# Kernel optimization log

Measured on AMD Instinct MI355X. Metric: run time of the kernel, lower is better.

Reference implementation:

```python
import jax, jax.numpy as jnp
import numpy as np

C = 512
K = 3
DIL = 1
EPS = 1e-6


def weight_quant(w):
    # BitNet b1.58 ternary quantization with straight-through estimator:
    # scale = mean(|w|); w_q = clamp(round(w/scale), -1, 1) * scale
    s = jnp.maximum(jnp.mean(jnp.abs(w)), 1e-5)
    q = jnp.clip(jnp.round(w / s), -1.0, 1.0) * s
    return w + jax.lax.stop_gradient(q - w)


def conv1d(x, w, b, padding, dilation):
    # x: [B, C, L], w: [O, I, K]
    y = jax.lax.conv_general_dilated(
        x, w, window_strides=(1,), padding=[(padding, padding)],
        rhs_dilation=(dilation,), dimension_numbers=("NCH", "OIH", "NCH"))
    return y + b[None, :, None]


def setup_inputs() -> dict:
    key = jax.random.key(0)
    k0, k1, k2, k3, k4 = jax.random.split(key, 5)
    fan_in = C * K
    lim = 1.0 / np.sqrt(fan_in)
    x = jax.random.normal(k0, (16, C, 4096), dtype=jnp.float32)
    w1 = jax.random.uniform(k1, (C, C, K), jnp.float32, -lim, lim)
    b1 = jax.random.uniform(k2, (C,), jnp.float32, -lim, lim)
    w2 = jax.random.uniform(k3, (C, C, K), jnp.float32, -lim, lim)
    b2 = jax.random.uniform(k4, (C,), jnp.float32, -lim, lim)
    g = jnp.ones((C,), dtype=jnp.float32)  # RMSNorm gain
    return {"x": x, "w1": w1, "b1": b1, "w2": w2, "b2": b2, "g": g}


def reference(x, w1, b1, w2, b2, g):
    residual = x
    # RMSNorm over channel axis (original transposes to [B,L,C], norms last dim)
    ms = jnp.mean(jnp.square(x), axis=1, keepdims=True)
    h = x * jax.lax.rsqrt(ms + EPS) * g[None, :, None]
    h = jax.nn.silu(h)
    p1 = (K * DIL - DIL) // 2
    h = conv1d(h, weight_quant(w1), b1, p1, DIL)
    h = jax.nn.silu(h)
    h = conv1d(h, weight_quant(w2), b2, K // 2, 1)
    return h + residual
```

## Files before the change

### kernel.cpp

```cpp
#include <hip/hip_runtime.h>

#define BATCH 16
#define CCH 512
#define LEN 4096
#define LPAD 4098

typedef unsigned short u16;
typedef __bf16 bf16x8 __attribute__((ext_vector_type(8)));
typedef float f32x4 __attribute__((ext_vector_type(4)));
typedef u16 u16x8 __attribute__((ext_vector_type(8)));
typedef u16 u16x4 __attribute__((ext_vector_type(4)));

__device__ __forceinline__ u16 f2bf(float f) {
    unsigned u = __float_as_uint(f);
    u = (u + 0x7fffu + ((u >> 16) & 1u)) >> 16;
    return (u16)u;
}
__device__ __forceinline__ float bf2f(u16 v) {
    return __uint_as_float(((unsigned)v) << 16);
}
__device__ __forceinline__ float silu_f(float v) {
    return v / (1.f + __expf(-v));
}
__device__ __forceinline__ void async16(const u16* g, u16* l) {
    __builtin_amdgcn_global_load_lds(
        (const __attribute__((address_space(1))) unsigned int*)g,
        (__attribute__((address_space(3))) unsigned int*)l, 16, 0, 0);
}

#define SBAR() __builtin_amdgcn_sched_barrier(0)
#define HWBAR() { SBAR(); __builtin_amdgcn_s_barrier(); SBAR(); }
#define WAIT_LGKM0() { asm volatile("s_waitcnt lgkmcnt(0)" ::: "memory"); SBAR(); }
#define WAIT_VM(n) { asm volatile("s_waitcnt vmcnt(" #n ")" ::: "memory"); SBAR(); }

__global__ __launch_bounds__(256)
void absmean_partial(const float* __restrict__ w1, const float* __restrict__ w2,
                     float* __restrict__ part) {
    const int tid = threadIdx.x;
    const int base = blockIdx.x * 3072;
    float s1 = 0.f, s2 = 0.f;
    for (int i = tid; i < 3072; i += 256) {
        s1 += fabsf(w1[base + i]);
        s2 += fabsf(w2[base + i]);
    }
    __shared__ float r1[256], r2[256];
    r1[tid] = s1; r2[tid] = s2;
    __syncthreads();
    for (int off = 128; off > 0; off >>= 1) {
        if (tid < off) { r1[tid] += r1[tid + off]; r2[tid] += r2[tid + off]; }
        __syncthreads();
    }
    if (tid == 0) { part[blockIdx.x] = r1[0]; part[256 + blockIdx.x] = r2[0]; }
}

__global__ __launch_bounds__(256)
void finalize_scale(const float* __restrict__ part, float* __restrict__ sv) {
    const int tid = threadIdx.x;
    __shared__ float r1[256], r2[256];
    r1[tid] = part[tid]; r2[tid] = part[256 + tid];
    __syncthreads();
    for (int off = 128; off > 0; off >>= 1) {
        if (tid < off) { r1[tid] += r1[tid + off]; r2[tid] += r2[tid + off]; }
        __syncthreads();
    }
    if (tid == 0) {
        sv[0] = fmaxf(r1[0] * (1.f / 786432.f), 1e-5f);
        sv[1] = fmaxf(r2[0] * (1.f / 786432.f), 1e-5f);
    }
}

__global__ __launch_bounds__(256)
void quantize_w(const float* __restrict__ w, const float* __restrict__ sv,
                int sidx, u16* __restrict__ wqt) {
    const int idx = blockIdx.x * 256 + threadIdx.x;
    const float s = sv[sidx];
    float q = rintf(w[idx] / s);
    q = fmaxf(-1.f, fminf(1.f, q));
    const int o   = idx / 1536;
    const int rem = idx - o * 1536;
    const int i   = rem / 3;
    const int k   = rem - i * 3;
    wqt[k * (CCH * CCH) + o * CCH + i] = f2bf(q);
}

__global__ __launch_bounds__(256)
void zero_pads(u16* __restrict__ h, u16* __restrict__ h1) {
    const int idx = blockIdx.x * 256 + threadIdx.x;
    const int b = idx >> 10;
    const int r = (idx >> 9) & 1;
    const int i = idx & 511;
    const size_t off = ((size_t)b * LPAD + (r ? (LPAD - 1) : 0)) * CCH + i;
    h[off] = 0;
    h1[off] = 0;
}

__global__ __launch_bounds__(256)
void rms_silu_transpose(const float* __restrict__ x, const float* __restrict__ g,
                        u16* __restrict__ h_t) {
    __shared__ u16   xt[CCH][33];
    __shared__ float red[8][32];
    __shared__ float rinv[32];
    const int tid = threadIdx.x;
    const int bb  = blockIdx.x >> 7;
    const int l0  = (blockIdx.x & 127) << 5;

    const size_t xbase = (size_t)bb * CCH * LEN + l0;
    {
        const int i_hi = tid >> 3;
        const int l4   = (tid & 7) << 2;
        #pragma unroll
        for (int it = 0; it < 16; ++it) {
            const int i = it * 32 + i_hi;
            const float4 v = *(const float4*)&x[xbase + (size_t)i * LEN + l4];
            xt[i][l4 + 0] = f2bf(v.x);
            xt[i][l4 + 1] = f2bf(v.y);
            xt[i][l4 + 2] = f2bf(v.z);
            xt[i][l4 + 3] = f2bf(v.w);
        }
    }
    __syncthreads();
    {
        const int l = tid & 31, seg = tid >> 5;
        const int ibeg = seg * 64;
        float ss = 0.f;
        #pragma unroll 8
        for (int i = ibeg; i < ibeg + 64; ++i) {
            const float v = bf2f(xt[i][l]);
            ss += v * v;
        }
        red[seg][l] = ss;
    }
    __syncthreads();
    if (tid < 32) {
        float tot = 0.f;
        #pragma unroll
        for (int k2 = 0; k2 < 8; ++k2) tot += red[k2][tid];
        rinv[tid] = rsqrtf(tot * (1.f / 512.f) + 1e-6f);
    }
    __syncthreads();
    {
        const int l  = tid >> 3;
        const int i0 = (tid & 7) << 6;
        const float ri = rinv[l];
        const size_t ob = ((size_t)bb * LPAD + l0 + l + 1) * CCH + i0;
        for (int ii = 0; ii < 64; ii += 8) {
            u16x8 ov;
            #pragma unroll
            for (int jj = 0; jj < 8; ++jj) {
                const int i = i0 + ii + jj;
                float v = bf2f(xt[i][l]) * ri * g[i];
                ov[jj] = f2bf(silu_f(v));
            }
            *(u16x8*)&h_t[ob + ii] = ov;
        }
    }
}

template<int EPI>
__global__ __launch_bounds__(256, 2)
void conv_gemm8(const u16* __restrict__ Bsrc, const u16* __restrict__ Wq,
                const float* __restrict__ sptr, const float* __restrict__ bias,
                const float* __restrict__ resid, u16* __restrict__ outb,
                float* __restrict__ outf) {
    extern __shared__ u16 lds[];
    const int tid  = threadIdx.x;
    const int lane = tid & 63;
    const int wave = tid >> 6;
    const int wm = wave >> 1;
    const int wn = wave & 1;

    const int wgid = (blockIdx.x & 7) * 128 + (blockIdx.x >> 3);
    const int mt = wgid & 1;
    const int nt = wgid >> 1;
    const int o0 = mt << 8;
    const int bb = nt >> 5;
    const int l0 = (nt & 31) << 7;

    const u16* aSrcBase = Wq + (size_t)(o0 + (tid >> 2)) * CCH + ((tid & 3) << 3);
    const u16* bSrcBase = Bsrc + ((size_t)bb * LPAD + l0 + (tid >> 2)) * CCH +
                          ((tid & 3) << 3);
    const int sdst = tid << 3;

    auto stage_full = [&](int pb, int t) {
        const int ks = t % 3;
        const int i0 = (t / 3) << 5;
        const u16* wsrc = aSrcBase + ks * (CCH * CCH) + i0;
        u16* const ad = &lds[pb * 12288 + sdst];
        #pragma unroll
        for (int j = 0; j < 4; ++j)
            async16(wsrc + j * 64 * CCH, ad + j * 2048);
        const u16* bsrc = bSrcBase + (size_t)ks * CCH + i0;
        u16* const bd = &lds[pb * 12288 + 8192 + sdst];
        #pragma unroll
        for (int j = 0; j < 2; ++j)
            async16(bsrc + (size_t)j * 64 * CCH, bd + j * 2048);
    };

    const int co   = (lane >> 4) << 3;
    const int aOff = wm * 4096 + (lane & 15) * 32 + co;
    const int bOff = 8192 + wn * 2048 + (lane & 15) * 32 + co;

    f32x4 acc[8][4];
    #pragma unroll
    for (int m = 0; m < 8; ++m)
        #pragma unroll
        for (int n = 0; n < 4; ++n)
            acc[m][n] = (f32x4){0.f, 0.f, 0.f, 0.f};

    stage_full(0, 0);
    stage_full(1, 1);
    WAIT_VM(6);
    HWBAR();

    int pb = 0;
    for (int t = 0; t < 48; ++t) {
        const bool full = (t < 46);
        if (full) {
            int nb = pb + 2; if (nb >= 3) nb -= 3;
            stage_full(nb, t + 2);
        }
        const int cb = pb * 12288;
        bf16x8 ar[8], br[4];
        #pragma unroll
        for (int m = 0; m < 8; ++m)
            ar[m] = *(const bf16x8*)&lds[cb + aOff + m * 512];
        #pragma unroll
        for (int n = 0; n < 4; ++n)
            br[n] = *(const bf16x8*)&lds[cb + bOff + n * 512];
        __builtin_amdgcn_s_setprio(1);
        #pragma unroll
        for (int m = 0; m < 8; ++m)
            #pragma unroll
            for (int n = 0; n < 4; ++n)
                acc[m][n] = __builtin_amdgcn_mfma_f32_16x16x32_bf16(
                    ar[m], br[n], acc[m][n], 0, 0, 0);
        __builtin_amdgcn_s_setprio(0);
        WAIT_LGKM0();
        if (full) { WAIT_VM(6); } else { WAIT_VM(0); }
        HWBAR();
        ++pb; if (pb == 3) pb = 0;
    }

    const float sc = sptr[0];

    if (EPI == 1) {
        #pragma unroll
        for (int m = 0; m < 8; ++m) {
            const int o_loc = wm * 128 + m * 16 + ((lane >> 4) << 2);
            const int ob = o0 + o_loc;
            const float b0 = bias[ob + 0], b1 = bias[ob + 1];
            const float b2 = bias[ob + 2], b3 = bias[ob + 3];
            #pragma unroll
            for (int n = 0; n < 4; ++n) {
                const int l_loc = wn * 64 + n * 16 + (lane & 15);
                const f32x4 a = acc[m][n];
                u16x4 ov;
                ov[0] = f2bf(silu_f(sc * a[0] + b0));
                ov[1] = f2bf(silu_f(sc * a[1] + b1));
                ov[2] = f2bf(silu_f(sc * a[2] + b2));
                ov[3] = f2bf(silu_f(sc * a[3] + b3));
                char* p = (char*)lds + l_loc * 512 +
                          (((unsigned)(o_loc << 1)) ^ ((l_loc & 7) << 4));
                *(u16x4*)p = ov;
            }
        }
        __syncthreads();
        const int oq = (tid & 3) << 3;
        #pragma unroll
        for (int pass = 0; pass < 2; ++pass) {
            const int lr = (tid >> 2) + pass * 64;
            u16* gdst = outb + ((size_t)bb * LPAD + l0 + lr + 1) * CCH + o0 + oq;
            char* srp = (char*)lds + lr * 512;
            const int swz2 = (lr & 7) << 4;
            #pragma unroll
            for (int c = 0; c < 8; ++c) {
                const uint4 v = *(const uint4*)(srp + ((oq * 2 + c * 64) ^ swz2));
                *(uint4*)(gdst + c * 32) = v;
            }
        }
    } else {
        const int lbase = l0 + wn * 64 + (lane & 15);
        const int obase = o0 + wm * 128 + ((lane >> 4) << 2);
        #pragma unroll
        for (int m = 0; m < 8; ++m) {
            const int ob = obase + m * 16;
            #pragma unroll
            for (int n = 0; n < 4; ++n) {
                const int l = lbase + n * 16;
                const f32x4 a = acc[m][n];
                #pragma unroll
                for (int jj = 0; jj < 4; ++jj) {
                    const size_t idx = ((size_t)bb * CCH + (ob + jj)) * LEN + l;
                    outf[idx] = sc * a[jj] + bias[ob + jj] + resid[idx];
                }
            }
        }
    }
}

extern "C" void kernel_launch(void* const* d_in, const int* in_sizes, int n_in,
                              void* d_out, int out_size, void* d_ws, size_t ws_size,
                              hipStream_t stream) {
    const float* x  = (const float*)d_in[0];
    const float* w1 = (const float*)d_in[1];
    const float* b1 = (const float*)d_in[2];
    const float* w2 = (const float*)d_in[3];
    const float* b2 = (const float*)d_in[4];
    const float* g  = (const float*)d_in[5];
    float* out = (float*)d_out;

    char* ws = (char*)d_ws;
    float* sv   = (float*)ws;
    float* part = (float*)(ws + 256);
    u16* wq1   = (u16*)(ws + 4096);
    u16* wq2   = (u16*)(ws + 4096 + 1572864);
    u16* h_t   = (u16*)(ws + 4096 + 2 * 1572864);
    u16* h1_t  = (u16*)(ws + 4096 + 2 * 1572864 + 67141632);

    hipFuncSetAttribute((const void*)conv_gemm8<1>,
                        hipFuncAttributeMaxDynamicSharedMemorySize, 73728);
    hipFuncSetAttribute((const void*)conv_gemm8<2>,
                        hipFuncAttributeMaxDynamicSharedMemorySize, 73728);

    absmean_partial<<<dim3(256), dim3(256), 0, stream>>>(w1, w2, part);
    finalize_scale<<<dim3(1), dim3(256), 0, stream>>>(part, sv);
    quantize_w<<<dim3(3072), dim3(256), 0, stream>>>(w1, sv, 0, wq1);
    quantize_w<<<dim3(3072), dim3(256), 0, stream>>>(w2, sv, 1, wq2);
    zero_pads<<<dim3(64), dim3(256), 0, stream>>>(h_t, h1_t);
    rms_silu_transpose<<<dim3(2048), dim3(256), 0, stream>>>(x, g, h_t);
    conv_gemm8<1><<<dim3(1024), dim3(256), 73728, stream>>>(h_t, wq1, sv, b1,
                                                            nullptr, h1_t, nullptr);
    conv_gemm8<2><<<dim3(1024), dim3(256), 73728, stream>>>(h1_t, wq2, sv + 1, b2,
                                                            x, nullptr, out);
}
```

Baseline: 331.6 us.

## Enlarge conv GEMM tile to 256x256 with 512 threads and swizzled LDS layout

The conv GEMM moves from 256-thread blocks with 256x128 tiles to 512-thread blocks with 256x256 tiles. This doubles the reuse of each staged weight tile and halves the number of workgroups. LDS staging now uses an XOR-swizzled layout to avoid bank conflicts, and the tail wait logic and epilogue store mapping are rewritten to match. The two weight-quantize launches are also fused into one. In exchange, occupancy drops to one large block per CU with 96KB of LDS in use, which may reduce latency hiding.

```diff
diff --git a/kernel.cpp b/kernel.cpp
--- a/kernel.cpp
+++ b/kernel.cpp
@@ -70,17 +70,20 @@
 }
 
 __global__ __launch_bounds__(256)
-void quantize_w(const float* __restrict__ w, const float* __restrict__ sv,
-                int sidx, u16* __restrict__ wqt) {
+void quantize_both(const float* __restrict__ w1, const float* __restrict__ w2,
+                   const float* __restrict__ sv,
+                   u16* __restrict__ wq1, u16* __restrict__ wq2) {
     const int idx = blockIdx.x * 256 + threadIdx.x;
-    const float s = sv[sidx];
-    float q = rintf(w[idx] / s);
-    q = fmaxf(-1.f, fminf(1.f, q));
+    const float s1 = sv[0], s2 = sv[1];
     const int o   = idx / 1536;
     const int rem = idx - o * 1536;
     const int i   = rem / 3;
     const int k   = rem - i * 3;
-    wqt[k * (CCH * CCH) + o * CCH + i] = f2bf(q);
+    const int dst = k * (CCH * CCH) + o * CCH + i;
+    float q1 = fmaxf(-1.f, fminf(1.f, rintf(w1[idx] / s1)));
+    float q2 = fmaxf(-1.f, fminf(1.f, rintf(w2[idx] / s2)));
+    wq1[dst] = f2bf(q1);
+    wq2[dst] = f2bf(q2);
 }
 
 __global__ __launch_bounds__(256)
@@ -157,48 +160,54 @@
 }
 
 template<int EPI>
-__global__ __launch_bounds__(256, 2)
-void conv_gemm8(const u16* __restrict__ Bsrc, const u16* __restrict__ Wq,
-                const float* __restrict__ sptr, const float* __restrict__ bias,
-                const float* __restrict__ resid, u16* __restrict__ outb,
-                float* __restrict__ outf) {
+__global__ __launch_bounds__(512)
+void conv_gemm12(const u16* __restrict__ Bsrc, const u16* __restrict__ Wq,
+                 const float* __restrict__ sptr, const float* __restrict__ bias,
+                 const float* __restrict__ resid, u16* __restrict__ outb,
+                 float* __restrict__ outf) {
     extern __shared__ u16 lds[];
     const int tid  = threadIdx.x;
     const int lane = tid & 63;
     const int wave = tid >> 6;
-    const int wm = wave >> 1;
-    const int wn = wave & 1;
-
-    const int wgid = (blockIdx.x & 7) * 128 + (blockIdx.x >> 3);
+    const int wm = wave >> 2;
+    const int wn = wave & 3;
+
+    const int wgid = (blockIdx.x & 7) * 64 + (blockIdx.x >> 3);
     const int mt = wgid & 1;
     const int nt = wgid >> 1;
     const int o0 = mt << 8;
-    const int bb = nt >> 5;
-    const int l0 = (nt & 31) << 7;
-
-    const u16* aSrcBase = Wq + (size_t)(o0 + (tid >> 2)) * CCH + ((tid & 3) << 3);
-    const u16* bSrcBase = Bsrc + ((size_t)bb * LPAD + l0 + (tid >> 2)) * CCH +
-                          ((tid & 3) << 3);
-    const int sdst = tid << 3;
-
-    auto stage_full = [&](int pb, int t) {
-        const int ks = t % 3;
-        const int i0 = (t / 3) << 5;
-        const u16* wsrc = aSrcBase + ks * (CCH * CCH) + i0;
-        u16* const ad = &lds[pb * 12288 + sdst];
-        #pragma unroll
-        for (int j = 0; j < 4; ++j)
-            async16(wsrc + j * 64 * CCH, ad + j * 2048);
-        const u16* bsrc = bSrcBase + (size_t)ks * CCH + i0;
-        u16* const bd = &lds[pb * 12288 + 8192 + sdst];
-        #pragma unroll
-        for (int j = 0; j < 2; ++j)
-            async16(bsrc + (size_t)j * 64 * CCH, bd + j * 2048);
+    const int bb = nt >> 4;
+    const int l0 = (nt & 15) << 8;
+
+    int rowj[2], coffj[2];
+    #pragma unroll
+    for (int j = 0; j < 2; ++j) {
+        const int s = tid + j * 512;
+        const int line = s >> 3;
+        const int val  = (s & 7) ^ (line & 7);
+        rowj[j]  = 2 * line + (val >> 2);
+        coffj[j] = (val & 3) << 3;
+    }
+    const u16* aS0 = Wq + (size_t)(o0 + rowj[0]) * CCH + coffj[0];
+    const u16* aS1 = Wq + (size_t)(o0 + rowj[1]) * CCH + coffj[1];
+    const u16* bS0 = Bsrc + ((size_t)bb * LPAD + l0 + rowj[0]) * CCH + coffj[0];
+    const u16* bS1 = Bsrc + ((size_t)bb * LPAD + l0 + rowj[1]) * CCH + coffj[1];
+
+    auto stage_full = [&](int pb, int ks2, int i02) {
+        const int aoff = ks2 * (CCH * CCH) + i02;
+        const int boff = ks2 * CCH + i02;
+        u16* const base = &lds[pb * 16384];
+        async16(aS0 + aoff, base + tid * 8);
+        async16(aS1 + aoff, base + 4096 + tid * 8);
+        async16(bS0 + boff, base + 8192 + tid * 8);
+        async16(bS1 + boff, base + 12288 + tid * 8);
     };
 
-    const int co   = (lane >> 4) << 3;
-    const int aOff = wm * 4096 + (lane & 15) * 32 + co;
-    const int bOff = 8192 + wn * 2048 + (lane & 15) * 32 + co;
+    const int q = lane >> 4;
+    const int halfl = (lane & 15) >> 1;
+    const int chunkp = (((lane & 1) << 2) | q) ^ halfl;
+    const int aBase = wm * 4096 + halfl * 64 + chunkp * 8;
+    const int bBase = 8192 + wn * 2048 + halfl * 64 + chunkp * 8;
 
     f32x4 acc[8][4];
     #pragma unroll
@@ -207,26 +216,27 @@
         for (int n = 0; n < 4; ++n)
             acc[m][n] = (f32x4){0.f, 0.f, 0.f, 0.f};
 
-    stage_full(0, 0);
-    stage_full(1, 1);
-    WAIT_VM(6);
+    stage_full(0, 0, 0);
+    stage_full(1, 1, 0);
+    WAIT_VM(4);
     HWBAR();
 
     int pb = 0;
+    int ks2 = 2, i02 = 0;
     for (int t = 0; t < 48; ++t) {
-        const bool full = (t < 46);
-        if (full) {
+        if (t < 46) {
             int nb = pb + 2; if (nb >= 3) nb -= 3;
-            stage_full(nb, t + 2);
-        }
-        const int cb = pb * 12288;
+            stage_full(nb, ks2, i02);
+            ++ks2; if (ks2 == 3) { ks2 = 0; i02 += 32; }
+        }
+        const int cb = pb * 16384;
         bf16x8 ar[8], br[4];
         #pragma unroll
         for (int m = 0; m < 8; ++m)
-            ar[m] = *(const bf16x8*)&lds[cb + aOff + m * 512];
+            ar[m] = *(const bf16x8*)&lds[cb + aBase + m * 512];
         #pragma unroll
         for (int n = 0; n < 4; ++n)
-            br[n] = *(const bf16x8*)&lds[cb + bOff + n * 512];
+            br[n] = *(const bf16x8*)&lds[cb + bBase + n * 512];
         __builtin_amdgcn_s_setprio(1);
         #pragma unroll
         for (int m = 0; m < 8; ++m)
@@ -236,7 +246,8 @@
                     ar[m], br[n], acc[m][n], 0, 0, 0);
         __builtin_amdgcn_s_setprio(0);
         WAIT_LGKM0();
-        if (full) { WAIT_VM(6); } else { WAIT_VM(0); }
+        if (t < 46) { WAIT_VM(4); }
+        else if (t == 46) { WAIT_VM(0); }
         HWBAR();
         ++pb; if (pb == 3) pb = 0;
     }
@@ -265,18 +276,15 @@
             }
         }
         __syncthreads();
-        const int oq = (tid & 3) << 3;
-        #pragma unroll
-        for (int pass = 0; pass < 2; ++pass) {
-            const int lr = (tid >> 2) + pass * 64;
-            u16* gdst = outb + ((size_t)bb * LPAD + l0 + lr + 1) * CCH + o0 + oq;
-            char* srp = (char*)lds + lr * 512;
-            const int swz2 = (lr & 7) << 4;
-            #pragma unroll
-            for (int c = 0; c < 8; ++c) {
-                const uint4 v = *(const uint4*)(srp + ((oq * 2 + c * 64) ^ swz2));
-                *(uint4*)(gdst + c * 32) = v;
-            }
+        const int row  = tid >> 1;
+        const int half = tid & 1;
+        u16* gdst = outb + ((size_t)bb * LPAD + l0 + row + 1) * CCH + o0 + half * 128;
+        char* srp = (char*)lds + row * 512;
+        const int swz2 = (row & 7) << 4;
+        #pragma unroll
+        for (int c = 0; c < 16; ++c) {
+            const uint4 v = *(const uint4*)(srp + ((half * 256 + c * 16) ^ swz2));
+            *(uint4*)(gdst + c * 8) = v;
         }
     } else {
         const int lbase = l0 + wn * 64 + (lane & 15);
@@ -317,19 +325,18 @@
     u16* h_t   = (u16*)(ws + 4096 + 2 * 1572864);
     u16* h1_t  = (u16*)(ws + 4096 + 2 * 1572864 + 67141632);
 
-    hipFuncSetAttribute((const void*)conv_gemm8<1>,
-                        hipFuncAttributeMaxDynamicSharedMemorySize, 73728);
-    hipFuncSetAttribute((const void*)conv_gemm8<2>,
-                        hipFuncAttributeMaxDynamicSharedMemorySize, 73728);
+    hipFuncSetAttribute((const void*)conv_gemm12<1>,
+                        hipFuncAttributeMaxDynamicSharedMemorySize, 131072);
+    hipFuncSetAttribute((const void*)conv_gemm12<2>,
+                        hipFuncAttributeMaxDynamicSharedMemorySize, 131072);
 
     absmean_partial<<<dim3(256), dim3(256), 0, stream>>>(w1, w2, part);
     finalize_scale<<<dim3(1), dim3(256), 0, stream>>>(part, sv);
-    quantize_w<<<dim3(3072), dim3(256), 0, stream>>>(w1, sv, 0, wq1);
-    quantize_w<<<dim3(3072), dim3(256), 0, stream>>>(w2, sv, 1, wq2);
+    quantize_both<<<dim3(3072), dim3(256), 0, stream>>>(w1, w2, sv, wq1, wq2);
     zero_pads<<<dim3(64), dim3(256), 0, stream>>>(h_t, h1_t);
     rms_silu_transpose<<<dim3(2048), dim3(256), 0, stream>>>(x, g, h_t);
-    conv_gemm8<1><<<dim3(1024), dim3(256), 73728, stream>>>(h_t, wq1, sv, b1,
-                                                            nullptr, h1_t, nullptr);
-    conv_gemm8<2><<<dim3(1024), dim3(256), 73728, stream>>>(h1_t, wq2, sv + 1, b2,
-                                                            x, nullptr, out);
-}
+    conv_gemm12<1><<<dim3(512), dim3(512), 131072, stream>>>(h_t, wq1, sv, b1,
+                                                             nullptr, h1_t, nullptr);
+    conv_gemm12<2><<<dim3(512), dim3(512), 131072, stream>>>(h1_t, wq2, sv + 1, b2,
+                                                             x, nullptr, out);
+}
```

Measured after the change: 343.3 us. +3.5%, slower.
